# Kernel tuning notes

Hardware: AMD Instinct MI355X
Metric: run time of the kernel (lower is better)

Reference implementation:

```python
import jax, jax.numpy as jnp
import numpy as np
import math

T = 2048
D_MODEL = 2048
N_H = 16
D_H = D_MODEL // N_H
EPS = 1e-5


def _rope_tables(t, d_h):
    # standard RoPE cos/sin tables, full head-dim layout matching rotate_half
    inv_freq = 1.0 / (10000.0 ** (jnp.arange(0, d_h // 2, dtype=jnp.float32) / (d_h // 2)))
    ang = jnp.arange(t, dtype=jnp.float32)[:, None] * inv_freq[None, :]  # (T, d_h/2)
    ang = jnp.concatenate([ang, ang], axis=-1)  # (T, d_h)
    return jnp.cos(ang), jnp.sin(ang)


def setup_inputs() -> dict:
    key = jax.random.key(0)
    kx, kq, kk, kv, ko = jax.random.split(key, 5)
    scale = 1.0 / math.sqrt(D_MODEL)
    cos, sin = _rope_tables(T, D_H)
    return {
        "x": jax.random.normal(kx, (T, D_MODEL), dtype=jnp.float32),
        "cos": cos,
        "sin": sin,
        "attention_mask": jnp.ones((T,), dtype=jnp.int32),
        "ln_w": jnp.ones((D_MODEL,), dtype=jnp.float32),
        "Wq": jax.random.normal(kq, (D_MODEL, D_MODEL), dtype=jnp.float32) * scale,
        "Wk": jax.random.normal(kk, (D_MODEL, D_MODEL), dtype=jnp.float32) * scale,
        "Wv": jax.random.normal(kv, (D_MODEL, D_MODEL), dtype=jnp.float32) * scale,
        "Wo": jax.random.normal(ko, (D_MODEL, D_MODEL), dtype=jnp.float32) * scale,
    }


def _rotate_half(x):
    x1, x2 = jnp.split(x, 2, axis=-1)
    return jnp.concatenate((-x2, x1), axis=-1)


def reference(x, cos, sin, attention_mask, ln_w, Wq, Wk, Wv, Wo):
    t = x.shape[0]
    # RMSNorm
    var = jnp.mean(x * x, axis=-1, keepdims=True)
    h = ln_w * x * jax.lax.rsqrt(var + EPS)
    # QKV projections (eqx Linear: weight @ x => x @ W.T), reshape to (n_h, T, d_h)
    q = (h @ Wq.T).reshape(t, N_H, D_H).transpose(1, 0, 2)
    k = (h @ Wk.T).reshape(t, N_H, D_H).transpose(1, 0, 2)
    v = (h @ Wv.T).reshape(t, N_H, D_H).transpose(1, 0, 2)
    # RoPE (cos/sin broadcast (T,d_h) -> (n_h,T,d_h))
    q = q * cos + _rotate_half(q) * sin
    k = k * cos + _rotate_half(k) * sin
    scores = jnp.einsum('hqd,hkd->hqk', q, k) / math.sqrt(D_H)
    causal = jnp.tril(jnp.ones((t, t), dtype=bool))[None]
    neg = jnp.finfo(scores.dtype).min
    am = attention_mask.astype(bool)
    allowed = causal & am[None, None, :]
    scores = jnp.where(allowed, scores, neg)
    scores = jnp.where(am[None, :, None], scores, neg)
    probs = jax.nn.softmax(scores, axis=-1)
    out = jnp.einsum('hqk,hkd->hqd', probs, v).transpose(1, 0, 2).reshape(t, -1)
    out = out @ Wo.T
    out = jnp.where(am[:, None], out, 0.0)
    return x + out
```

## Files before the change

kernel.cpp:

```cpp
#include <hip/hip_runtime.h>
#include <stdint.h>

#define TS 2048
#define DM 2048
#define NH 16
#define DH 128

typedef unsigned short u16t;
typedef __attribute__((ext_vector_type(8))) short short8;
typedef __attribute__((ext_vector_type(4))) float f32x4;
typedef __attribute__((ext_vector_type(4))) unsigned int u32x4;

__device__ __forceinline__ float bf2f(u16t b) {
  return __uint_as_float(((unsigned int)b) << 16);
}
__device__ __forceinline__ u16t f2bf(float f) {
  unsigned int u = __float_as_uint(f);
  u += 0x7FFFu + ((u >> 16) & 1u);
  return (u16t)(u >> 16);
}

__device__ __forceinline__ void async_copy16(const u16t* g, u16t* l) {
  __builtin_amdgcn_global_load_lds((const __attribute__((address_space(1))) void*)g,
                                   (__attribute__((address_space(3))) void*)l, 16, 0, 0);
}

#define DPP_ROR_F(x, n) __uint_as_float(__builtin_amdgcn_update_dpp( \
    0, (int)__float_as_uint(x), 0x120 | (n), 0xF, 0xF, true))

__device__ __forceinline__ float row16_max(float x) {
  x = fmaxf(x, DPP_ROR_F(x, 8));
  x = fmaxf(x, DPP_ROR_F(x, 4));
  x = fmaxf(x, DPP_ROR_F(x, 2));
  x = fmaxf(x, DPP_ROR_F(x, 1));
  return x;
}
__device__ __forceinline__ float row16_sum(float x) {
  x += DPP_ROR_F(x, 8);
  x += DPP_ROR_F(x, 4);
  x += DPP_ROR_F(x, 2);
  x += DPP_ROR_F(x, 1);
  return x;
}

__global__ __launch_bounds__(256) void cast_rms_kernel(const float* __restrict__ W0,
                                                       const float* __restrict__ W1,
                                                       const float* __restrict__ W2,
                                                       const float* __restrict__ W3,
                                                       u16t* __restrict__ outw,
                                                       const float* __restrict__ x,
                                                       const float* __restrict__ lnw,
                                                       u16t* __restrict__ h) {
  if (blockIdx.x < 16384) {
    const int idx = blockIdx.x * 256 + threadIdx.x;
    const int mat = idx >> 20;
    const size_t off = (size_t)(idx & 0xFFFFF) * 4;
    const float* W = (mat == 0) ? W0 : (mat == 1) ? W1 : (mat == 2) ? W2 : W3;
    const f32x4 v = *(const f32x4*)(W + off);
    size_t dstoff = off;
    if (mat < 2) {
      const int row = (int)(off >> 11);
      const int col = (int)(off & 2047);
      const int d = row & 127;
      const int e = d & 63;
      const int p = ((e >> 4) * 32 + (e & 15)) + ((d >> 6) << 4);
      dstoff = ((size_t)((row & ~127) | p) << 11) | (size_t)col;
    }
    union { u16t s[4]; uint64_t u; } o;
#pragma unroll
    for (int i = 0; i < 4; ++i) o.s[i] = f2bf(v[i]);
    *(uint64_t*)(outw + (size_t)mat * (DM * DM) + dstoff) = o.u;
    return;
  }
  const int row = blockIdx.x - 16384;
  const int tid = threadIdx.x;
  const float* xr = x + (size_t)row * DM + tid * 8;
  f32x4 v0 = *(const f32x4*)(xr);
  f32x4 v1 = *(const f32x4*)(xr + 4);
  float f[8];
#pragma unroll
  for (int i = 0; i < 4; ++i) { f[i] = v0[i]; f[i + 4] = v1[i]; }
  float ss = 0.f;
#pragma unroll
  for (int i = 0; i < 8; ++i) ss += f[i] * f[i];
#pragma unroll
  for (int off = 1; off < 64; off <<= 1) ss += __shfl_xor(ss, off, 64);
  __shared__ float wsum[4];
  if ((tid & 63) == 0) wsum[tid >> 6] = ss;
  __syncthreads();
  float tot = wsum[0] + wsum[1] + wsum[2] + wsum[3];
  float rs = rsqrtf(tot * (1.0f / DM) + 1e-5f);
  f32x4 w0 = *(const f32x4*)(lnw + tid * 8);
  f32x4 w1 = *(const f32x4*)(lnw + tid * 8 + 4);
  u32x4 o;
#pragma unroll
  for (int i = 0; i < 4; ++i) {
    unsigned int lo = f2bf(f[2 * i]     * ((2 * i     < 4) ? w0[2 * i]     : w1[2 * i - 4]) * rs);
    unsigned int hi = f2bf(f[2 * i + 1] * ((2 * i + 1 < 4) ? w0[2 * i + 1] : w1[2 * i - 3]) * rs);
    o[i] = lo | (hi << 16);
  }
  *(u32x4*)(h + (size_t)row * DM + tid * 8) = o;
}

template <int MODE>
__global__ __launch_bounds__(256) void gemm_bt(
    const u16t* __restrict__ A,
    const u16t* __restrict__ B0, const u16t* __restrict__ B1, const u16t* __restrict__ B2,
    u16t* __restrict__ Cq, u16t* __restrict__ Ck, u16t* __restrict__ Cv,
    const float* __restrict__ cosb, const float* __restrict__ sinb,
    const float* __restrict__ xres, const int* __restrict__ am, float* __restrict__ out) {
  __shared__ u16t Alds[128 * 32];
  __shared__ u16t Blds[128 * 32];
  const int tid  = threadIdx.x;
  const int wave = tid >> 6;
  const int lane = tid & 63;
  const int lin  = blockIdx.y * 16 + blockIdx.x;
  const int xcd  = lin & 7;
  const int sidx = lin >> 3;
  const int m0 = (sidx & 15) * 128;
  const int n0 = ((xcd << 1) | (sidx >> 4)) * 128;
  const int mat = (MODE == 0) ? blockIdx.z : 0;
  const u16t* B = (MODE == 0) ? (mat == 0 ? B0 : (mat == 1 ? B1 : B2)) : B0;

  const f32x4 fzero = {0.f, 0.f, 0.f, 0.f};
  f32x4 acc[4][4];
#pragma unroll
  for (int i = 0; i < 4; ++i)
#pragma unroll
    for (int j = 0; j < 4; ++j) acc[i][j] = fzero;

  const int lr = lane >> 2;
  const int lc = lane & 3;
  const int mw = (wave >> 1) * 64;
  const int nw = (wave & 1) * 64;
  const int quad = lane >> 4;
  const int c16  = lane & 15;

  for (int k0 = 0; k0 < DM; k0 += 32) {
    __syncthreads();
#pragma unroll
    for (int c = 0; c < 2; ++c) {
      const int ch = wave * 2 + c;
      const int r  = ch * 16 + lr;
      async_copy16(A + (size_t)(m0 + r) * DM + k0 + lc * 8, Alds + ch * 512);
      async_copy16(B + (size_t)(n0 + r) * DM + k0 + lc * 8, Blds + ch * 512);
    }
    __syncthreads();
    short8 af[4], bfr[4];
#pragma unroll
    for (int mt = 0; mt < 4; ++mt)
      af[mt] = *(const short8*)(Alds + (mw + mt * 16 + c16) * 32 + quad * 8);
#pragma unroll
    for (int nt = 0; nt < 4; ++nt)
      bfr[nt] = *(const short8*)(Blds + (nw + nt * 16 + c16) * 32 + quad * 8);
#pragma unroll
    for (int mt = 0; mt < 4; ++mt)
#pragma unroll
      for (int nt = 0; nt < 4; ++nt)
        acc[mt][nt] = __builtin_amdgcn_mfma_f32_16x16x32_bf16(af[mt], bfr[nt], acc[mt][nt], 0, 0, 0);
  }

  if (MODE == 1) {
#pragma unroll
    for (int mt = 0; mt < 4; ++mt) {
#pragma unroll
      for (int r = 0; r < 4; ++r) {
        const int row = m0 + mw + mt * 16 + quad * 4 + r;
        const float mk = (am[row] != 0) ? 1.f : 0.f;
        const size_t base = (size_t)row * DM;
#pragma unroll
        for (int nt = 0; nt < 4; ++nt) {
          const int col = n0 + nw + nt * 16 + c16;
          out[base + col] = xres[base + col] + mk * acc[mt][nt][r];
        }
      }
    }
    return;
  }

  if (mat == 2) {
#pragma unroll
    for (int mt = 0; mt < 4; ++mt) {
#pragma unroll
      for (int r = 0; r < 4; ++r) {
        const int row = m0 + mw + mt * 16 + quad * 4 + r;
#pragma unroll
        for (int nt = 0; nt < 4; ++nt) {
          const int col = n0 + nw + nt * 16 + c16;
          Cv[(size_t)col * TS + row] = f2bf(acc[mt][nt][r]);
        }
      }
    }
    return;
  }

  u16t* C = mat ? Ck : Cq;
#pragma unroll
  for (int mt = 0; mt < 4; ++mt) {
#pragma unroll
    for (int r = 0; r < 4; ++r) {
      const int row = m0 + mw + mt * 16 + quad * 4 + r;
      const size_t base = (size_t)row * DM;
#pragma unroll
      for (int ntp = 0; ntp < 4; ntp += 2) {
        const int col = n0 + nw + ntp * 16 + c16;
        const int p = col & 127;
        const int dorig = (p >> 5) * 16 + c16;
        const float cv = cosb[row * DH + dorig];
        const float sv = sinb[row * DH + dorig];
        const float x1 = acc[mt][ntp][r];
        const float x2 = acc[mt][ntp + 1][r];
        C[base + col]      = f2bf(x1 * cv - x2 * sv);
        C[base + col + 16] = f2bf(x2 * cv + x1 * sv);
      }
    }
  }
}

__global__ __launch_bounds__(256) void attn_kernel(const u16t* __restrict__ Q,
                                                   const u16t* __restrict__ K,
                                                   const u16t* __restrict__ Vt,
                                                   const int* __restrict__ am,
                                                   u16t* __restrict__ O) {
  __shared__ u16t Klds[128 * 128];
  __shared__ u16t Vlds[128 * 128];
  __shared__ u16t Plds[4][2048];
  const int wave = threadIdx.x >> 6;
  const int lane = threadIdx.x & 63;
  const int x    = blockIdx.x;
  const int half = x >> 8;
  const int idx  = x & 255;
  const int head = idx & (NH - 1);
  const int grp  = idx >> 4;
  const int qt   = half ? grp : (TS / 64 - 1 - grp);
  const int q0   = qt * 64 + wave * 16;
  const int quad = lane >> 4;
  const int c16  = lane & 15;
  const u16t* Qh  = Q + head * DH;
  const u16t* Kh  = K + head * DH;
  const u16t* Vth = Vt + (size_t)head * DH * TS;
  u16t* Pw = Plds[wave];

  const int row_s = (lane >> 4);
  const int g_s   = (lane & 15);

  short8 qf[4];
#pragma unroll
  for (int dc = 0; dc < 4; ++dc)
    qf[dc] = *(const short8*)(Qh + (size_t)(q0 + c16) * DM + dc * 32 + quad * 8);

  const f32x4 fzero = {0.f, 0.f, 0.f, 0.f};
  float m_run[4], l_run[4];
  f32x4 o_acc[8];
#pragma unroll
  for (int r = 0; r < 4; ++r) { m_run[r] = -1e30f; l_run[r] = 0.f; }
#pragma unroll
  for (int nt = 0; nt < 8; ++nt) o_acc[nt] = fzero;

  const float scale = 0.08838834764831845f;
  const int ntiles = (qt * 64 + 191) >> 7;

  for (int kt = 0; kt < ntiles; ++kt) {
    const int k0 = kt * 128;
    __syncthreads();
#pragma unroll
    for (int c = 0; c < 8; ++c) {
      const int ch = wave * 8 + c;
      const int r  = 4 * ch + row_s;
      const int g  = g_s ^ (r & 15);
      async_copy16(Kh + (size_t)(k0 + r) * DM + g * 8, Klds + ch * 512);
      async_copy16(Vth + (size_t)r * TS + k0 + g * 8, Vlds + ch * 512);
    }
    __syncthreads();

    f32x4 s[8];
#pragma unroll
    for (int ns = 0; ns < 8; ++ns) {
      f32x4 sa = fzero;
      const int rr = ns * 16 + c16;
#pragma unroll
      for (int dc = 0; dc < 4; ++dc) {
        short8 kf = *(const short8*)(Klds + rr * 128 + (((dc * 4 + quad) ^ c16) * 8));
        sa = __builtin_amdgcn_mfma_f32_16x16x32_bf16(qf[dc], kf, sa, 0, 0, 0);
      }
      s[ns] = sa;
    }

    float pv[8][4], tmax[4];
#pragma unroll
    for (int r = 0; r < 4; ++r) tmax[r] = -1e30f;
#pragma unroll
    for (int ns = 0; ns < 8; ++ns) {
      const int key = k0 + ns * 16 + c16;
      const bool kok = (am[key] != 0);
#pragma unroll
      for (int r = 0; r < 4; ++r) {
        const int qrow = q0 + quad * 4 + r;
        float v = s[ns][r] * scale;
        if (key > qrow || !kok) v = -1e30f;
        pv[ns][r] = v;
        tmax[r] = fmaxf(tmax[r], v);
      }
    }
    float alpha[4], rsum[4];
#pragma unroll
    for (int r = 0; r < 4; ++r) {
      const float mn = fmaxf(m_run[r], row16_max(tmax[r]));
      alpha[r] = __expf(m_run[r] - mn);
      m_run[r] = mn;
      float rs = 0.f;
#pragma unroll
      for (int ns = 0; ns < 8; ++ns) {
        const float e = __expf(pv[ns][r] - mn);
        pv[ns][r] = e;
        rs += e;
      }
      rsum[r] = row16_sum(rs);
      l_run[r] = l_run[r] * alpha[r] + rsum[r];
    }

#pragma unroll
    for (int ns = 0; ns < 8; ++ns)
#pragma unroll
      for (int r = 0; r < 4; ++r)
        Pw[(ns >> 1) * 512 + (quad * 4 + r) * 32 + (ns & 1) * 16 + c16] = f2bf(pv[ns][r]);
    asm volatile("s_waitcnt lgkmcnt(0)" ::: "memory");
    short8 pf[4];
#pragma unroll
    for (int c = 0; c < 4; ++c)
      pf[c] = *(const short8*)(Pw + c * 512 + c16 * 32 + quad * 8);

#pragma unroll
    for (int nt = 0; nt < 8; ++nt)
#pragma unroll
      for (int r = 0; r < 4; ++r) o_acc[nt][r] *= alpha[r];
#pragma unroll
    for (int nt = 0; nt < 8; ++nt) {
      const int rr = nt * 16 + c16;
#pragma unroll
      for (int c = 0; c < 4; ++c) {
        short8 vf = *(const short8*)(Vlds + rr * 128 + (((c * 4 + quad) ^ c16) * 8));
        o_acc[nt] = __builtin_amdgcn_mfma_f32_16x16x32_bf16(pf[c], vf, o_acc[nt], 0, 0, 0);
      }
    }
  }

#pragma unroll
  for (int r = 0; r < 4; ++r) {
    const float inv = 1.0f / fmaxf(l_run[r], 1e-20f);
    const int qrow = q0 + quad * 4 + r;
#pragma unroll
    for (int nt = 0; nt < 8; ++nt)
      O[(size_t)qrow * DM + head * DH + nt * 16 + c16] = f2bf(o_acc[nt][r] * inv);
  }
}

extern "C" void kernel_launch(void* const* d_in, const int* in_sizes, int n_in,
                              void* d_out, int out_size, void* d_ws, size_t ws_size,
                              hipStream_t stream) {
  const float* x    = (const float*)d_in[0];
  const float* cosb = (const float*)d_in[1];
  const float* sinb = (const float*)d_in[2];
  const int*   am   = (const int*)d_in[3];
  const float* lnw  = (const float*)d_in[4];
  const float* Wq   = (const float*)d_in[5];
  const float* Wk   = (const float*)d_in[6];
  const float* Wv   = (const float*)d_in[7];
  const float* Wo   = (const float*)d_in[8];
  float* out = (float*)d_out;

  u16t* h    = (u16t*)d_ws;
  u16t* Q    = h + (size_t)TS * DM;
  u16t* K    = Q + (size_t)TS * DM;
  u16t* Vt   = K + (size_t)TS * DM;
  u16t* attn = Vt + (size_t)TS * DM;
  u16t* Wb   = attn + (size_t)TS * DM;
  u16t* Wqb = Wb;
  u16t* Wkb = Wb + (size_t)DM * DM;
  u16t* Wvb = Wb + 2 * (size_t)DM * DM;
  u16t* Wob = Wb + 3 * (size_t)DM * DM;

  cast_rms_kernel<<<16384 + TS, 256, 0, stream>>>(Wq, Wk, Wv, Wo, Wb, x, lnw, h);
  gemm_bt<0><<<dim3(16, 16, 3), 256, 0, stream>>>(h, Wqb, Wkb, Wvb, Q, K, Vt,
                                                  cosb, sinb, nullptr, nullptr, nullptr);
  attn_kernel<<<NH * (TS / 64), 256, 0, stream>>>(Q, K, Vt, am, attn);
  gemm_bt<1><<<dim3(16, 16, 1), 256, 0, stream>>>(attn, Wob, nullptr, nullptr,
                                                  nullptr, nullptr, nullptr,
                                                  nullptr, nullptr, x, am, out);
}
```

Baseline: 310.3 us.

## Rewrite GEMMs with 256x256 double-buffered tiles and split-K output projection

Replaces the 128x128, 32-deep, single-buffered GEMM with a 512-thread 256x256 tile kernel using 64-deep K steps. It double-buffers LDS with async global-to-LDS copies, XOR-swizzles the LDS layout to avoid bank conflicts, and raises wave priority around the MFMA blocks. The output projection now uses 4-way split-K across 256 workgroups, writing bf16 partials into reused workspace buffers that a new combine kernel sums with the residual and mask. The aim is more data reuse per tile and overlap of loads with compute. In exchange it adds an extra kernel launch, extra memory traffic for the partials, and bf16 rounding of each partial sum.

```diff
diff --git a/kernel.cpp b/kernel.cpp
--- a/kernel.cpp
+++ b/kernel.cpp
@@ -10,6 +10,7 @@
 typedef __attribute__((ext_vector_type(8))) short short8;
 typedef __attribute__((ext_vector_type(4))) float f32x4;
 typedef __attribute__((ext_vector_type(4))) unsigned int u32x4;
+typedef __attribute__((ext_vector_type(4))) unsigned short u16x4;
 
 __device__ __forceinline__ float bf2f(u16t b) {
   return __uint_as_float(((unsigned int)b) << 16);
@@ -103,109 +104,141 @@
 }
 
 template <int MODE>
-__global__ __launch_bounds__(256) void gemm_bt(
+__global__ __launch_bounds__(512, 2) void gemm8(
     const u16t* __restrict__ A,
     const u16t* __restrict__ B0, const u16t* __restrict__ B1, const u16t* __restrict__ B2,
     u16t* __restrict__ Cq, u16t* __restrict__ Ck, u16t* __restrict__ Cv,
-    const float* __restrict__ cosb, const float* __restrict__ sinb,
-    const float* __restrict__ xres, const int* __restrict__ am, float* __restrict__ out) {
-  __shared__ u16t Alds[128 * 32];
-  __shared__ u16t Blds[128 * 32];
+    u16t* __restrict__ P0, u16t* __restrict__ P1,
+    u16t* __restrict__ P2, u16t* __restrict__ P3,
+    const float* __restrict__ cosb, const float* __restrict__ sinb) {
+  __shared__ u16t Ab[2][256 * 64];
+  __shared__ u16t Bb[2][256 * 64];
   const int tid  = threadIdx.x;
   const int wave = tid >> 6;
   const int lane = tid & 63;
-  const int lin  = blockIdx.y * 16 + blockIdx.x;
-  const int xcd  = lin & 7;
-  const int sidx = lin >> 3;
-  const int m0 = (sidx & 15) * 128;
-  const int n0 = ((xcd << 1) | (sidx >> 4)) * 128;
-  const int mat = (MODE == 0) ? blockIdx.z : 0;
-  const u16t* B = (MODE == 0) ? (mat == 0 ? B0 : (mat == 1 ? B1 : B2)) : B0;
-
-  const f32x4 fzero = {0.f, 0.f, 0.f, 0.f};
-  f32x4 acc[4][4];
-#pragma unroll
-  for (int i = 0; i < 4; ++i)
-#pragma unroll
-    for (int j = 0; j < 4; ++j) acc[i][j] = fzero;
-
-  const int lr = lane >> 2;
-  const int lc = lane & 3;
-  const int mw = (wave >> 1) * 64;
-  const int nw = (wave & 1) * 64;
   const int quad = lane >> 4;
   const int c16  = lane & 15;
-
-  for (int k0 = 0; k0 < DM; k0 += 32) {
-    __syncthreads();
-#pragma unroll
-    for (int c = 0; c < 2; ++c) {
-      const int ch = wave * 2 + c;
-      const int r  = ch * 16 + lr;
-      async_copy16(A + (size_t)(m0 + r) * DM + k0 + lc * 8, Alds + ch * 512);
-      async_copy16(B + (size_t)(n0 + r) * DM + k0 + lc * 8, Blds + ch * 512);
-    }
-    __syncthreads();
-    short8 af[4], bfr[4];
-#pragma unroll
-    for (int mt = 0; mt < 4; ++mt)
-      af[mt] = *(const short8*)(Alds + (mw + mt * 16 + c16) * 32 + quad * 8);
-#pragma unroll
-    for (int nt = 0; nt < 4; ++nt)
-      bfr[nt] = *(const short8*)(Blds + (nw + nt * 16 + c16) * 32 + quad * 8);
-#pragma unroll
-    for (int mt = 0; mt < 4; ++mt)
-#pragma unroll
-      for (int nt = 0; nt < 4; ++nt)
-        acc[mt][nt] = __builtin_amdgcn_mfma_f32_16x16x32_bf16(af[mt], bfr[nt], acc[mt][nt], 0, 0, 0);
+  const int h7   = c16 & 7;
+  const int wm   = wave >> 2;
+  const int wn   = wave & 3;
+  const int nwg  = gridDim.x;
+  const int bid  = blockIdx.x;
+  const int wgid = (bid & 7) * (nwg >> 3) + (bid >> 3);
+  const int mat  = wgid >> 6;
+  const int rem  = wgid & 63;
+  const int m0   = (rem & 7) * 256;
+  const int n0   = ((rem >> 3) & 7) * 256;
+  const u16t* B  = (MODE == 0) ? (mat == 0 ? B0 : (mat == 1 ? B1 : B2)) : B0;
+  const int kbeg = (MODE == 0) ? 0 : mat * (DM / 4);
+  const int NT   = (MODE == 0) ? (DM / 64) : (DM / 4 / 64);
+
+  const int srow = lane >> 3;
+  const int sg   = (lane & 7) ^ srow;
+  auto stage = [&](int d, int k0) {
+    const size_t koff = (size_t)k0 + sg * 8;
+#pragma unroll
+    for (int c = 0; c < 4; ++c) {
+      const int rb = wave * 32 + c * 8;
+      async_copy16(A + (size_t)(m0 + rb + srow) * DM + koff, &Ab[d][rb * 64]);
+      async_copy16(B + (size_t)(n0 + rb + srow) * DM + koff, &Bb[d][rb * 64]);
+    }
+  };
+
+  const f32x4 fzero = {0.f, 0.f, 0.f, 0.f};
+  f32x4 acc[8][4];
+#pragma unroll
+  for (int i = 0; i < 8; ++i)
+#pragma unroll
+    for (int j = 0; j < 4; ++j) acc[i][j] = fzero;
+
+  stage(0, kbeg);
+  stage(1, kbeg + 64);
+
+  for (int kt = 0; kt < NT; ++kt) {
+    const int cur = kt & 1;
+    if (kt < NT - 1) { asm volatile("s_waitcnt vmcnt(8)" ::: "memory"); }
+    else             { asm volatile("s_waitcnt vmcnt(0)" ::: "memory"); }
+    __builtin_amdgcn_s_barrier();
+    const u16t* Abuf = Ab[cur];
+    const u16t* Bbuf = Bb[cur];
+    short8 bf[4];
+#pragma unroll
+    for (int ph = 0; ph < 4; ++ph) {
+      const int hh = ph & 1;
+      const int ks = ph >> 1;
+      short8 af[4];
+#pragma unroll
+      for (int i = 0; i < 4; ++i) {
+        const int row = wm * 128 + (hh * 4 + i) * 16 + c16;
+        af[i] = *(const short8*)(Abuf + row * 64 + (((ks * 4 + quad) ^ h7) * 8));
+      }
+      if (hh == 0) {
+#pragma unroll
+        for (int nt = 0; nt < 4; ++nt) {
+          const int row = wn * 64 + nt * 16 + c16;
+          bf[nt] = *(const short8*)(Bbuf + row * 64 + (((ks * 4 + quad) ^ h7) * 8));
+        }
+      }
+      __builtin_amdgcn_s_barrier();
+      asm volatile("s_waitcnt lgkmcnt(0)" ::: "memory");
+      __builtin_amdgcn_sched_barrier(0);
+      __builtin_amdgcn_s_setprio(1);
+#pragma unroll
+      for (int i = 0; i < 4; ++i)
+#pragma unroll
+        for (int nt = 0; nt < 4; ++nt)
+          acc[hh * 4 + i][nt] =
+              __builtin_amdgcn_mfma_f32_16x16x32_bf16(af[i], bf[nt], acc[hh * 4 + i][nt], 0, 0, 0);
+      __builtin_amdgcn_s_setprio(0);
+      __builtin_amdgcn_s_barrier();
+    }
+    if (kt + 2 < NT) stage(cur, kbeg + (kt + 2) * 64);
   }
 
   if (MODE == 1) {
-#pragma unroll
-    for (int mt = 0; mt < 4; ++mt) {
+    u16t* P = (mat == 0) ? P0 : (mat == 1) ? P1 : (mat == 2) ? P2 : P3;
+#pragma unroll
+    for (int mt = 0; mt < 8; ++mt) {
 #pragma unroll
       for (int r = 0; r < 4; ++r) {
-        const int row = m0 + mw + mt * 16 + quad * 4 + r;
-        const float mk = (am[row] != 0) ? 1.f : 0.f;
+        const int row = m0 + wm * 128 + mt * 16 + quad * 4 + r;
         const size_t base = (size_t)row * DM;
 #pragma unroll
         for (int nt = 0; nt < 4; ++nt) {
-          const int col = n0 + nw + nt * 16 + c16;
-          out[base + col] = xres[base + col] + mk * acc[mt][nt][r];
+          const int col = n0 + wn * 64 + nt * 16 + c16;
+          P[base + col] = f2bf(acc[mt][nt][r]);
         }
       }
     }
     return;
   }
-
   if (mat == 2) {
 #pragma unroll
-    for (int mt = 0; mt < 4; ++mt) {
+    for (int mt = 0; mt < 8; ++mt) {
 #pragma unroll
       for (int r = 0; r < 4; ++r) {
-        const int row = m0 + mw + mt * 16 + quad * 4 + r;
+        const int row = m0 + wm * 128 + mt * 16 + quad * 4 + r;
 #pragma unroll
         for (int nt = 0; nt < 4; ++nt) {
-          const int col = n0 + nw + nt * 16 + c16;
+          const int col = n0 + wn * 64 + nt * 16 + c16;
           Cv[(size_t)col * TS + row] = f2bf(acc[mt][nt][r]);
         }
       }
     }
     return;
   }
-
   u16t* C = mat ? Ck : Cq;
 #pragma unroll
-  for (int mt = 0; mt < 4; ++mt) {
+  for (int mt = 0; mt < 8; ++mt) {
 #pragma unroll
     for (int r = 0; r < 4; ++r) {
-      const int row = m0 + mw + mt * 16 + quad * 4 + r;
+      const int row = m0 + wm * 128 + mt * 16 + quad * 4 + r;
       const size_t base = (size_t)row * DM;
 #pragma unroll
       for (int ntp = 0; ntp < 4; ntp += 2) {
-        const int col = n0 + nw + ntp * 16 + c16;
+        const int col = n0 + wn * 64 + ntp * 16 + c16;
         const int p = col & 127;
-        const int dorig = (p >> 5) * 16 + c16;
+        const int dorig = ((p >> 5) << 4) + c16;
         const float cv = cosb[row * DH + dorig];
         const float sv = sinb[row * DH + dorig];
         const float x1 = acc[mt][ntp][r];
@@ -215,6 +248,28 @@
       }
     }
   }
+}
+
+__global__ __launch_bounds__(256) void combine4_kernel(const u16t* __restrict__ P0,
+                                                       const u16t* __restrict__ P1,
+                                                       const u16t* __restrict__ P2,
+                                                       const u16t* __restrict__ P3,
+                                                       const float* __restrict__ x,
+                                                       const int* __restrict__ am,
+                                                       float* __restrict__ out) {
+  const size_t idx = ((size_t)blockIdx.x * 256 + threadIdx.x) * 4;
+  const int row = (int)(idx >> 11);
+  const float mk = (am[row] != 0) ? 1.f : 0.f;
+  const u16x4 a = *(const u16x4*)(P0 + idx);
+  const u16x4 b = *(const u16x4*)(P1 + idx);
+  const u16x4 c = *(const u16x4*)(P2 + idx);
+  const u16x4 d = *(const u16x4*)(P3 + idx);
+  const f32x4 xr = *(const f32x4*)(x + idx);
+  f32x4 o;
+#pragma unroll
+  for (int i = 0; i < 4; ++i)
+    o[i] = xr[i] + mk * ((bf2f(a[i]) + bf2f(b[i])) + (bf2f(c[i]) + bf2f(d[i])));
+  *(f32x4*)(out + idx) = o;
 }
 
 __global__ __launch_bounds__(256) void attn_kernel(const u16t* __restrict__ Q,
@@ -381,10 +436,11 @@
   u16t* Wob = Wb + 3 * (size_t)DM * DM;
 
   cast_rms_kernel<<<16384 + TS, 256, 0, stream>>>(Wq, Wk, Wv, Wo, Wb, x, lnw, h);
-  gemm_bt<0><<<dim3(16, 16, 3), 256, 0, stream>>>(h, Wqb, Wkb, Wvb, Q, K, Vt,
-                                                  cosb, sinb, nullptr, nullptr, nullptr);
+  gemm8<0><<<192, 512, 0, stream>>>(h, Wqb, Wkb, Wvb, Q, K, Vt,
+                                    nullptr, nullptr, nullptr, nullptr, cosb, sinb);
   attn_kernel<<<NH * (TS / 64), 256, 0, stream>>>(Q, K, Vt, am, attn);
-  gemm_bt<1><<<dim3(16, 16, 1), 256, 0, stream>>>(attn, Wob, nullptr, nullptr,
-                                                  nullptr, nullptr, nullptr,
-                                                  nullptr, nullptr, x, am, out);
-}
+  gemm8<1><<<256, 512, 0, stream>>>(attn, Wob, nullptr, nullptr,
+                                    nullptr, nullptr, nullptr,
+                                    h, Q, K, Vt, nullptr, nullptr);
+  combine4_kernel<<<(TS * DM / 4) / 256, 256, 0, stream>>>(h, Q, K, Vt, x, am, out);
+}
```

After: 299.8 us. 1.03x faster.
